# Performance work log

Measured on AMD Instinct MI355X. Metric: run time of the kernel, lower is better.

Reference implementation:

```python
import jax, jax.numpy as jnp
import numpy as np

N_ITER = 64   # projected-subgradient iterations of the batched DRO QP solver
LR0 = 0.05    # base step size (diminishing 1/sqrt(t))


def project_simplex(v):
    # Euclidean projection onto {z >= 0, sum z = 1} (sort-based, O(n log n))
    n = v.shape[0]
    u = jnp.sort(v)[::-1]
    css = jnp.cumsum(u) - 1.0
    k = jnp.arange(1, n + 1, dtype=v.dtype)
    cond = (u - css / k) > 0          # prefix-true pattern
    idx = jnp.sum(cond.astype(jnp.int32)) - 1
    theta = jnp.take(css, idx) / jnp.take(k, idx)
    return jnp.maximum(v - theta, 0.0)


def _dro_obj(z, c, lam, ep, y_hat, rho):
    # Tractable TV-DRO counterpart (Ben-Tal et al. 2013) with eta and obj_aux
    # eliminated analytically:
    #   obj_i* = max(-lam, u_i - eta),  u_i = (ep_i.z - c)^2
    #   feasibility: eta >= max_i u_i - lam; objective nondecreasing in eta
    #   => eta* = max_i u_i - lam
    s = ep @ z - c                     # (n_obs,)
    u = s * s
    umax = jnp.max(u)
    inner = jnp.mean(jnp.maximum(-lam, u - umax + lam))
    return (umax - lam) + rho * lam + inner - jnp.dot(y_hat, z)


_grad_obj = jax.grad(_dro_obj, argnums=(0, 1, 2))


def _solve_one(y_hat, ep, rho):
    # Projected subgradient descent on (z in simplex, c free, lam >= 0)
    n_y = y_hat.shape[0]
    z0 = jnp.full((n_y,), 1.0 / n_y, y_hat.dtype)
    c0 = jnp.mean(ep @ z0)
    lam0 = jnp.asarray(1.0, y_hat.dtype)

    def step(carry, t):
        z, c, lam = carry
        gz, gc, glam = _grad_obj(z, c, lam, ep, y_hat, rho)
        lr = LR0 / jnp.sqrt(t + 1.0)
        z = project_simplex(z - lr * gz)
        c = c - lr * gc
        lam = jnp.maximum(lam - lr * glam, 0.0)
        return (z, c, lam), None

    (z, _, _), _ = jax.lax.scan(step, (z0, c0, lam0),
                                jnp.arange(N_ITER, dtype=y_hat.dtype))
    return z


def setup_inputs() -> dict:
    key = jax.random.key(0)
    kx, ky, kw, kb = jax.random.split(key, 4)
    n_obs, n_x, n_y = 2048, 128, 64
    X = jax.random.normal(kx, (n_obs, n_x), jnp.float32)
    Y = jax.random.normal(ky, (n_obs, n_y), jnp.float32)
    W = jax.random.normal(kw, (n_y, n_x), jnp.float32) / np.sqrt(n_x).astype(np.float32)
    b = jax.random.normal(kb, (n_y,), jnp.float32) * 0.01
    rho = jnp.array([0.1], jnp.float32)
    return {"X": X, "Y": Y, "rho": rho, "W": W, "b": b}


def reference(X, Y, rho, W, b):
    # prediction layer: per-sample linear predict (vectorized over n_obs)
    Y_hat = X @ W.T + b                        # (n_obs, n_y)
    ep = Y - Y_hat                             # residuals, shared by all solves
    # batched DRO solve: one convex problem per scenario y_hat_t (vmapped)
    Z_star = jax.vmap(lambda yh: _solve_one(yh, ep, rho[0]))(Y_hat)
    Z_star = jax.lax.stop_gradient(Z_star)     # torch code detaches z_t
    return Z_star, Y_hat
```

## Files before the change

### kernel.cpp

```cpp
#include <hip/hip_runtime.h>

#define NOBS 2048
#define NX   128
#define NY   64
#define BS   8
#define NT   1024
#define NWAVE (NT / 64)
#define NITER 64

template <int CTRL>
__device__ __forceinline__ float dpp_f(float x) {
    return __int_as_float(__builtin_amdgcn_update_dpp(
        0, __float_as_int(x), CTRL, 0xf, 0xf, true));
}
__device__ __forceinline__ float wave_sum64(float v) {
    v += dpp_f<0x111>(v);
    v += dpp_f<0x112>(v);
    v += dpp_f<0x114>(v);
    v += dpp_f<0x118>(v);
    v += dpp_f<0x142>(v);
    v += dpp_f<0x143>(v);
    return v;
}
__device__ __forceinline__ float wave_max64_nonneg(float v) {
    v = fmaxf(v, dpp_f<0x111>(v));
    v = fmaxf(v, dpp_f<0x112>(v));
    v = fmaxf(v, dpp_f<0x114>(v));
    v = fmaxf(v, dpp_f<0x118>(v));
    v = fmaxf(v, dpp_f<0x142>(v));
    v = fmaxf(v, dpp_f<0x143>(v));
    return v;
}

__global__ __launch_bounds__(256) void prep_kernel(
    const float* __restrict__ X, const float* __restrict__ Y,
    const float* __restrict__ W, const float* __restrict__ b,
    float* __restrict__ yhat_out, float* __restrict__ ep, float* __restrict__ epsum)
{
    __shared__ float Xs[4][NX];
    const int t = threadIdx.x;
    const int row0 = blockIdx.x * 4;
    for (int f = t; f < 4 * NX; f += 256)
        Xs[f >> 7][f & 127] = X[(row0 + (f >> 7)) * NX + (f & 127)];
    __syncthreads();

    const int k = t & 63;
    const int r = t >> 6;
    const float4* W4 = reinterpret_cast<const float4*>(W + k * NX);
    const float4* X4 = reinterpret_cast<const float4*>(&Xs[r][0]);
    float acc = 0.f;
    #pragma unroll
    for (int x = 0; x < NX / 4; ++x) {
        float4 wv = W4[x];
        float4 xv = X4[x];
        acc += wv.x * xv.x + wv.y * xv.y + wv.z * xv.z + wv.w * xv.w;
    }
    const float yh = acc + b[k];
    const int i = row0 + r;
    yhat_out[i * NY + k] = yh;
    const float e = Y[i * NY + k] - yh;
    ep[i * NY + k] = e;

    float se = wave_sum64(e);
    if ((t & 63) == 63) atomicAdd(epsum, se);
}

__global__ __launch_bounds__(NT, 4) void solve_kernel(
    const float* __restrict__ ep, const float* __restrict__ yhat,
    const float* __restrict__ epsum, const float* __restrict__ rho_p,
    float* __restrict__ zout)
{
    __shared__ float Zs[BS][NY];
    __shared__ float Yh[BS][NY];
    __shared__ float V[NOBS][BS];
    __shared__ float Rpart[NWAVE][NY][BS];
    __shared__ float Rr[NY][BS];
    __shared__ float redBuf[NWAVE][32];
    __shared__ float scal[32];
    __shared__ float umaxS[BS], cS[BS], lamS[BS], gcS[BS], glamS[BS], wAS[BS];

    const int t = threadIdx.x;
    const int lane = t & 63;
    const int wv = t >> 6;
    const int sc0 = blockIdx.x * BS;
    const float rho = rho_p[0];

    if (t < BS * NY) {
        const int j = t >> 6, k = t & 63;
        Yh[j][k] = yhat[(sc0 + j) * NY + k];
        Zs[j][k] = 1.0f / 64.0f;
    }
    if (t < BS) {
        cS[t] = epsum[0] * (1.0f / 131072.0f);
        lamS[t] = 1.0f;
    }
    __syncthreads();

    const int i0 = t;
    const int i1 = t + NT;
    const float4* ep4 = reinterpret_cast<const float4*>(ep);

    for (int it = 0; it < NITER; ++it) {
        const float lr = 0.05f / sqrtf((float)it + 1.0f);

        float s0[BS], s1[BS];
        #pragma unroll
        for (int j = 0; j < BS; ++j) { s0[j] = 0.f; s1[j] = 0.f; }
        #pragma unroll 4
        for (int k4 = 0; k4 < NY / 4; ++k4) {
            const float4 ea = ep4[i0 * (NY / 4) + k4];
            const float4 eb = ep4[i1 * (NY / 4) + k4];
            #pragma unroll
            for (int j = 0; j < BS; ++j) {
                const float4 zv = *reinterpret_cast<const float4*>(&Zs[j][k4 * 4]);
                s0[j] += ea.x * zv.x + ea.y * zv.y + ea.z * zv.z + ea.w * zv.w;
                s1[j] += eb.x * zv.x + eb.y * zv.y + eb.z * zv.z + eb.w * zv.w;
            }
        }
        float lamR[BS];
        #pragma unroll
        for (int j = 0; j < BS; ++j) {
            const float cj = cS[j];
            lamR[j] = lamS[j];
            s0[j] -= cj; s1[j] -= cj;
        }

        #pragma unroll
        for (int j = 0; j < BS; ++j) {
            float pm = fmaxf(s0[j] * s0[j], s1[j] * s1[j]);
            pm = wave_max64_nonneg(pm);
            if (lane == 63) redBuf[wv][j] = pm;
        }
        __syncthreads();
        if (t < BS) {
            float m = redBuf[0][t];
            #pragma unroll
            for (int w = 1; w < NWAVE; ++w) m = fmaxf(m, redBuf[w][t]);
            umaxS[t] = m;
        }
        __syncthreads();

        #pragma unroll
        for (int j = 0; j < BS; ++j) {
            const float um = umaxS[j], lm = lamR[j];
            float pa = 0.f, pe = 0.f, pas = 0.f, pes = 0.f;
            {
                const float s = s0[j], u = s * s;
                const float x = (u - um) + lm;
                const float a = (x > -lm) ? 1.0f : ((x == -lm) ? 0.5f : 0.0f);
                const float e = (u == um) ? 1.0f : 0.0f;
                pa += a; pe += e; pas += a * s; pes += e * s;
            }
            {
                const float s = s1[j], u = s * s;
                const float x = (u - um) + lm;
                const float a = (x > -lm) ? 1.0f : ((x == -lm) ? 0.5f : 0.0f);
                const float e = (u == um) ? 1.0f : 0.0f;
                pa += a; pe += e; pas += a * s; pes += e * s;
            }
            pa = wave_sum64(pa); pe = wave_sum64(pe);
            pas = wave_sum64(pas); pes = wave_sum64(pes);
            if (lane == 63) {
                redBuf[wv][j] = pa;       redBuf[wv][8 + j] = pe;
                redBuf[wv][16 + j] = pas; redBuf[wv][24 + j] = pes;
            }
        }
        __syncthreads();
        if (t < 32) {
            float ssum = 0.f;
            #pragma unroll
            for (int w = 0; w < NWAVE; ++w) ssum += redBuf[w][t];
            scal[t] = ssum;
        }
        __syncthreads();
        if (t < BS) {
            const int j = t;
            const float sumA = scal[j], sumEq = scal[8 + j];
            const float sumAS = scal[16 + j], sumEqS = scal[24 + j];
            const float abar = sumA * (1.0f / (float)NOBS);
            const float wA = (1.0f - abar) / sumEq;
            wAS[j] = wA;
            gcS[j] = -2.0f * (sumAS * (1.0f / (float)NOBS) + wA * sumEqS);
            glamS[j] = (rho - 2.0f) + 2.0f * abar;
        }
        __syncthreads();

        {
            float v0[BS], v1[BS];
            #pragma unroll
            for (int j = 0; j < BS; ++j) {
                const float um = umaxS[j], lm = lamR[j], wA = wAS[j];
                {
                    const float s = s0[j], u = s * s;
                    const float x = (u - um) + lm;
                    const float a = (x > -lm) ? 1.0f : ((x == -lm) ? 0.5f : 0.0f);
                    const float e = (u == um) ? 1.0f : 0.0f;
                    v0[j] = (a * (1.0f / (float)NOBS) + e * wA) * s;
                }
                {
                    const float s = s1[j], u = s * s;
                    const float x = (u - um) + lm;
                    const float a = (x > -lm) ? 1.0f : ((x == -lm) ? 0.5f : 0.0f);
                    const float e = (u == um) ? 1.0f : 0.0f;
                    v1[j] = (a * (1.0f / (float)NOBS) + e * wA) * s;
                }
            }
            *reinterpret_cast<float4*>(&V[i0][0]) = make_float4(v0[0], v0[1], v0[2], v0[3]);
            *reinterpret_cast<float4*>(&V[i0][4]) = make_float4(v0[4], v0[5], v0[6], v0[7]);
            *reinterpret_cast<float4*>(&V[i1][0]) = make_float4(v1[0], v1[1], v1[2], v1[3]);
            *reinterpret_cast<float4*>(&V[i1][4]) = make_float4(v1[4], v1[5], v1[6], v1[7]);
        }
        __syncthreads();

        {
            float rp[BS];
            #pragma unroll
            for (int j = 0; j < BS; ++j) rp[j] = 0.f;
            const int ibeg = wv * (NOBS / NWAVE);
            #pragma unroll 4
            for (int ii = 0; ii < NOBS / NWAVE; ++ii) {
                const int i = ibeg + ii;
                const float e = ep[i * NY + lane];
                const float4 va = *reinterpret_cast<const float4*>(&V[i][0]);
                const float4 vb = *reinterpret_cast<const float4*>(&V[i][4]);
                rp[0] += e * va.x; rp[1] += e * va.y; rp[2] += e * va.z; rp[3] += e * va.w;
                rp[4] += e * vb.x; rp[5] += e * vb.y; rp[6] += e * vb.z; rp[7] += e * vb.w;
            }
            *reinterpret_cast<float4*>(&Rpart[wv][lane][0]) = make_float4(rp[0], rp[1], rp[2], rp[3]);
            *reinterpret_cast<float4*>(&Rpart[wv][lane][4]) = make_float4(rp[4], rp[5], rp[6], rp[7]);
        }
        __syncthreads();
        if (t < NY * BS) {
            const int k = t >> 3, j = t & 7;
            float ssum = 0.f;
            #pragma unroll
            for (int w = 0; w < NWAVE; ++w) ssum += Rpart[w][k][j];
            Rr[k][j] = ssum;
        }
        __syncthreads();

        if (wv < BS) {
            const int j = wv, k = lane;
            const float r = Rr[k][j];
            const float gz = 2.0f * r - Yh[j][k];
            const float vz = Zs[j][k] - lr * gz;

            float sv = vz;
            #pragma unroll
            for (int sz = 2; sz <= 64; sz <<= 1) {
                #pragma unroll
                for (int st = sz >> 1; st > 0; st >>= 1) {
                    const float other = __shfl_xor(sv, st, 64);
                    const bool desc = ((lane & sz) == 0);
                    const bool lower = ((lane & st) == 0);
                    const float mx = fmaxf(sv, other), mn = fminf(sv, other);
                    sv = (lower == desc) ? mx : mn;
                }
            }
            float css = sv;
            #pragma unroll
            for (int off = 1; off < 64; off <<= 1) {
                const float nb = __shfl_up(css, off, 64);
                if (lane >= off) css += nb;
            }
            css -= 1.0f;
            const bool cond = (sv - css / (float)(lane + 1)) > 0.0f;
            const unsigned long long bal = __ballot(cond);
            const int idx = __popcll(bal) - 1;
            const float cssIdx = __shfl(css, idx, 64);
            const float theta = cssIdx / (float)(idx + 1);
            Zs[j][k] = fmaxf(vz - theta, 0.0f);
            if (lane == 0) {
                cS[j] = cS[j] - lr * gcS[j];
                lamS[j] = fmaxf(lamS[j] - lr * glamS[j], 0.0f);
            }
        }
        __syncthreads();
    }

    if (t < BS * NY) {
        const int j = t >> 6, k = t & 63;
        zout[(sc0 + j) * NY + k] = Zs[j][k];
    }
}

extern "C" void kernel_launch(void* const* d_in, const int* in_sizes, int n_in,
                              void* d_out, int out_size, void* d_ws, size_t ws_size,
                              hipStream_t stream) {
    const float* X   = (const float*)d_in[0];
    const float* Y   = (const float*)d_in[1];
    const float* rho = (const float*)d_in[2];
    const float* W   = (const float*)d_in[3];
    const float* b   = (const float*)d_in[4];

    float* out   = (float*)d_out;
    float* zout  = out;
    float* yhat  = out + NOBS * NY;
    float* ep    = (float*)d_ws;
    float* epsum = ep + NOBS * NY;

    hipMemsetAsync(epsum, 0, sizeof(float), stream);
    prep_kernel<<<NOBS / 4, 256, 0, stream>>>(X, Y, W, b, yhat, ep, epsum);
    solve_kernel<<<NOBS / BS, NT, 0, stream>>>(ep, yhat, epsum, rho, zout);
}
```

Baseline: 2.162 ms.

## Use LDS atomics for block reductions and register-tile the ep^T·V gradient

Per-wave max and sum partials now go straight into shared accumulators through LDS atomicMax/atomicAdd, which removes two barriers and the serial cross-wave reduction passes in each iteration. Every thread recomputes wA from the shared sums itself, and the accumulators are reset during the Rr reduction phase. The ep^T·V gradient loop is restructured so each lane loads float4 ep rows and keeps 4x8 accumulators, and partials are combined with cross-lane shuffles. z and y_hat stay in registers for the projection step. The changes add register pressure and rely on the atomic float-as-int max being valid for non-negative values.

Result: slower. 5.667 ms (+162.1%).

```diff
diff --git a/kernel.cpp b/kernel.cpp
--- a/kernel.cpp
+++ b/kernel.cpp
@@ -70,14 +70,13 @@
     const float* __restrict__ epsum, const float* __restrict__ rho_p,
     float* __restrict__ zout)
 {
-    __shared__ float Zs[BS][NY];
-    __shared__ float Yh[BS][NY];
     __shared__ float V[NOBS][BS];
     __shared__ float Rpart[NWAVE][NY][BS];
     __shared__ float Rr[NY][BS];
-    __shared__ float redBuf[NWAVE][32];
+    __shared__ float Zs[BS][NY];
     __shared__ float scal[32];
-    __shared__ float umaxS[BS], cS[BS], lamS[BS], gcS[BS], glamS[BS], wAS[BS];
+    __shared__ int   umaxI[BS];
+    __shared__ float cS[BS], lamS[BS], gcS[BS], glamS[BS];
 
     const int t = threadIdx.x;
     const int lane = t & 63;
@@ -85,12 +84,14 @@
     const int sc0 = blockIdx.x * BS;
     const float rho = rho_p[0];
 
-    if (t < BS * NY) {
-        const int j = t >> 6, k = t & 63;
-        Yh[j][k] = yhat[(sc0 + j) * NY + k];
-        Zs[j][k] = 1.0f / 64.0f;
-    }
+    float zReg = 1.0f / 64.0f;
+    float yhReg = 0.0f;
+    if (wv < BS) yhReg = yhat[(sc0 + wv) * NY + lane];
+
+    if (t < BS * NY) Zs[t >> 6][t & 63] = 1.0f / 64.0f;
+    if (t < 32) scal[t] = 0.0f;
     if (t < BS) {
+        umaxI[t] = 0;
         cS[t] = epsum[0] * (1.0f / 131072.0f);
         lamS[t] = 1.0f;
     }
@@ -99,6 +100,8 @@
     const int i0 = t;
     const int i1 = t + NT;
     const float4* ep4 = reinterpret_cast<const float4*>(ep);
+    const float4* epA = ep4 + i0 * (NY / 4);
+    const float4* epB = ep4 + i1 * (NY / 4);
 
     for (int it = 0; it < NITER; ++it) {
         const float lr = 0.05f / sqrtf((float)it + 1.0f);
@@ -108,8 +111,8 @@
         for (int j = 0; j < BS; ++j) { s0[j] = 0.f; s1[j] = 0.f; }
         #pragma unroll 4
         for (int k4 = 0; k4 < NY / 4; ++k4) {
-            const float4 ea = ep4[i0 * (NY / 4) + k4];
-            const float4 eb = ep4[i1 * (NY / 4) + k4];
+            const float4 ea = epA[k4];
+            const float4 eb = epB[k4];
             #pragma unroll
             for (int j = 0; j < BS; ++j) {
                 const float4 zv = *reinterpret_cast<const float4*>(&Zs[j][k4 * 4]);
@@ -129,80 +132,71 @@
         for (int j = 0; j < BS; ++j) {
             float pm = fmaxf(s0[j] * s0[j], s1[j] * s1[j]);
             pm = wave_max64_nonneg(pm);
-            if (lane == 63) redBuf[wv][j] = pm;
-        }
-        __syncthreads();
-        if (t < BS) {
-            float m = redBuf[0][t];
-            #pragma unroll
-            for (int w = 1; w < NWAVE; ++w) m = fmaxf(m, redBuf[w][t]);
-            umaxS[t] = m;
-        }
-        __syncthreads();
+            if (lane == 63) atomicMax(&umaxI[j], __float_as_int(pm));
+        }
+        __syncthreads();
+
+        float um[BS];
+        #pragma unroll
+        for (int j = 0; j < BS; ++j) um[j] = __int_as_float(umaxI[j]);
 
         #pragma unroll
         for (int j = 0; j < BS; ++j) {
-            const float um = umaxS[j], lm = lamR[j];
-            float pa = 0.f, pe = 0.f, pas = 0.f, pes = 0.f;
+            const float umj = um[j], lm = lamR[j];
+            float pa, pe, pas, pes;
             {
                 const float s = s0[j], u = s * s;
-                const float x = (u - um) + lm;
+                const float x = (u - umj) + lm;
                 const float a = (x > -lm) ? 1.0f : ((x == -lm) ? 0.5f : 0.0f);
-                const float e = (u == um) ? 1.0f : 0.0f;
-                pa += a; pe += e; pas += a * s; pes += e * s;
+                const float e = (u == umj) ? 1.0f : 0.0f;
+                pa = a; pe = e; pas = a * s; pes = e * s;
             }
             {
                 const float s = s1[j], u = s * s;
-                const float x = (u - um) + lm;
+                const float x = (u - umj) + lm;
                 const float a = (x > -lm) ? 1.0f : ((x == -lm) ? 0.5f : 0.0f);
-                const float e = (u == um) ? 1.0f : 0.0f;
+                const float e = (u == umj) ? 1.0f : 0.0f;
                 pa += a; pe += e; pas += a * s; pes += e * s;
             }
             pa = wave_sum64(pa); pe = wave_sum64(pe);
             pas = wave_sum64(pas); pes = wave_sum64(pes);
             if (lane == 63) {
-                redBuf[wv][j] = pa;       redBuf[wv][8 + j] = pe;
-                redBuf[wv][16 + j] = pas; redBuf[wv][24 + j] = pes;
-            }
-        }
-        __syncthreads();
-        if (t < 32) {
-            float ssum = 0.f;
-            #pragma unroll
-            for (int w = 0; w < NWAVE; ++w) ssum += redBuf[w][t];
-            scal[t] = ssum;
-        }
-        __syncthreads();
+                atomicAdd(&scal[j], pa);       atomicAdd(&scal[8 + j], pe);
+                atomicAdd(&scal[16 + j], pas); atomicAdd(&scal[24 + j], pes);
+            }
+        }
+        __syncthreads();
+
+        float wA[BS];
+        #pragma unroll
+        for (int j = 0; j < BS; ++j) {
+            const float abar = scal[j] * (1.0f / (float)NOBS);
+            wA[j] = (1.0f - abar) / scal[8 + j];
+        }
         if (t < BS) {
-            const int j = t;
-            const float sumA = scal[j], sumEq = scal[8 + j];
-            const float sumAS = scal[16 + j], sumEqS = scal[24 + j];
-            const float abar = sumA * (1.0f / (float)NOBS);
-            const float wA = (1.0f - abar) / sumEq;
-            wAS[j] = wA;
-            gcS[j] = -2.0f * (sumAS * (1.0f / (float)NOBS) + wA * sumEqS);
-            glamS[j] = (rho - 2.0f) + 2.0f * abar;
-        }
-        __syncthreads();
-
+            const float abar = scal[t] * (1.0f / (float)NOBS);
+            const float wAt = (1.0f - abar) / scal[8 + t];
+            gcS[t] = -2.0f * (scal[16 + t] * (1.0f / (float)NOBS) + wAt * scal[24 + t]);
+            glamS[t] = (rho - 2.0f) + 2.0f * abar;
+        }
         {
             float v0[BS], v1[BS];
             #pragma unroll
             for (int j = 0; j < BS; ++j) {
-                const float um = umaxS[j], lm = lamR[j], wA = wAS[j];
+                const float umj = um[j], lm = lamR[j], wAj = wA[j];
                 {
                     const float s = s0[j], u = s * s;
-                    const float x = (u - um) + lm;
+                    const float x = (u - umj) + lm;
                     const float a = (x > -lm) ? 1.0f : ((x == -lm) ? 0.5f : 0.0f);
-                    const float e = (u == um) ? 1.0f : 0.0f;
-                    v0[j] = (a * (1.0f / (float)NOBS) + e * wA) * s;
+                    const float e = (u == umj) ? 1.0f : 0.0f;
+                    v0[j] = (a * (1.0f / (float)NOBS) + e * wAj) * s;
                 }
                 {
                     const float s = s1[j], u = s * s;
-                    const float x = (u - um) + lm;
+                    const float x = (u - umj) + lm;
                     const float a = (x > -lm) ? 1.0f : ((x == -lm) ? 0.5f : 0.0f);
-                    const float e = (u == um) ? 1.0f : 0.0f;
-                    v1[j] = (a * (1.0f / (float)NOBS) + e * wA) * s;
+                    const float e = (u == umj) ? 1.0f : 0.0f;
+                    v1[j] = (a * (1.0f / (float)NOBS) + e * wAj) * s;
                 }
             }
             *reinterpret_cast<float4*>(&V[i0][0]) = make_float4(v0[0], v0[1], v0[2], v0[3]);
@@ -213,37 +207,71 @@
         __syncthreads();
 
         {
-            float rp[BS];
-            #pragma unroll
-            for (int j = 0; j < BS; ++j) rp[j] = 0.f;
-            const int ibeg = wv * (NOBS / NWAVE);
-            #pragma unroll 4
-            for (int ii = 0; ii < NOBS / NWAVE; ++ii) {
-                const int i = ibeg + ii;
-                const float e = ep[i * NY + lane];
-                const float4 va = *reinterpret_cast<const float4*>(&V[i][0]);
-                const float4 vb = *reinterpret_cast<const float4*>(&V[i][4]);
-                rp[0] += e * va.x; rp[1] += e * va.y; rp[2] += e * va.z; rp[3] += e * va.w;
-                rp[4] += e * vb.x; rp[5] += e * vb.y; rp[6] += e * vb.z; rp[7] += e * vb.w;
-            }
-            *reinterpret_cast<float4*>(&Rpart[wv][lane][0]) = make_float4(rp[0], rp[1], rp[2], rp[3]);
-            *reinterpret_cast<float4*>(&Rpart[wv][lane][4]) = make_float4(rp[4], rp[5], rp[6], rp[7]);
-        }
-        __syncthreads();
+            const int sub = lane >> 4;
+            const int kq  = lane & 15;
+            float rp0[BS], rp1[BS], rp2[BS], rp3[BS];
+            #pragma unroll
+            for (int j = 0; j < BS; ++j) { rp0[j] = 0.f; rp1[j] = 0.f; rp2[j] = 0.f; rp3[j] = 0.f; }
+
+            const int rbase = wv * (NOBS / NWAVE) + sub;
+            const float4* vp = reinterpret_cast<const float4*>(&V[rbase][0]);
+            #pragma unroll
+            for (int c8 = 0; c8 < 8; ++c8) {
+                const float4* epc = ep4 + (rbase + c8 * 16) * (NY / 4) + kq;
+                #pragma unroll
+                for (int u = 0; u < 4; ++u) {
+                    const int ii = c8 * 4 + u;
+                    const float4 e4 = epc[u * 64];
+                    const float4 va = vp[ii * 8];
+                    const float4 vb = vp[ii * 8 + 1];
+                    rp0[0] += e4.x * va.x; rp0[1] += e4.x * va.y; rp0[2] += e4.x * va.z; rp0[3] += e4.x * va.w;
+                    rp0[4] += e4.x * vb.x; rp0[5] += e4.x * vb.y; rp0[6] += e4.x * vb.z; rp0[7] += e4.x * vb.w;
+                    rp1[0] += e4.y * va.x; rp1[1] += e4.y * va.y; rp1[2] += e4.y * va.z; rp1[3] += e4.y * va.w;
+                    rp1[4] += e4.y * vb.x; rp1[5] += e4.y * vb.y; rp1[6] += e4.y * vb.z; rp1[7] += e4.y * vb.w;
+                    rp2[0] += e4.z * va.x; rp2[1] += e4.z * va.y; rp2[2] += e4.z * va.z; rp2[3] += e4.z * va.w;
+                    rp2[4] += e4.z * vb.x; rp2[5] += e4.z * vb.y; rp2[6] += e4.z * vb.z; rp2[7] += e4.z * vb.w;
+                    rp3[0] += e4.w * va.x; rp3[1] += e4.w * va.y; rp3[2] += e4.w * va.z; rp3[3] += e4.w * va.w;
+                    rp3[4] += e4.w * vb.x; rp3[5] += e4.w * vb.y; rp3[6] += e4.w * vb.z; rp3[7] += e4.w * vb.w;
+                }
+            }
+            #pragma unroll
+            for (int j = 0; j < BS; ++j) {
+                float a0 = rp0[j]; a0 += __shfl_xor(a0, 16, 64); a0 += __shfl_xor(a0, 32, 64); rp0[j] = a0;
+                float a1 = rp1[j]; a1 += __shfl_xor(a1, 16, 64); a1 += __shfl_xor(a1, 32, 64); rp1[j] = a1;
+                float a2 = rp2[j]; a2 += __shfl_xor(a2, 16, 64); a2 += __shfl_xor(a2, 32, 64); rp2[j] = a2;
+                float a3 = rp3[j]; a3 += __shfl_xor(a3, 16, 64); a3 += __shfl_xor(a3, 32, 64); rp3[j] = a3;
+            }
+            float w[BS];
+            #pragma unroll
+            for (int j = 0; j < BS; ++j) {
+                const float t01 = (sub & 1) ? rp1[j] : rp0[j];
+                const float t23 = (sub & 1) ? rp3[j] : rp2[j];
+                w[j] = (sub & 2) ? t23 : t01;
+            }
+            float* dst = &Rpart[wv][4 * kq + sub][0];
+            *reinterpret_cast<float4*>(dst)     = make_float4(w[0], w[1], w[2], w[3]);
+            *reinterpret_cast<float4*>(dst + 4) = make_float4(w[4], w[5], w[6], w[7]);
+        }
+        __syncthreads();
+
         if (t < NY * BS) {
             const int k = t >> 3, j = t & 7;
             float ssum = 0.f;
             #pragma unroll
             for (int w = 0; w < NWAVE; ++w) ssum += Rpart[w][k][j];
             Rr[k][j] = ssum;
+        } else if (t < NY * BS + 32) {
+            scal[t - NY * BS] = 0.0f;
+        } else if (t < NY * BS + 32 + BS) {
+            umaxI[t - NY * BS - 32] = 0;
         }
         __syncthreads();
 
         if (wv < BS) {
             const int j = wv, k = lane;
             const float r = Rr[k][j];
-            const float gz = 2.0f * r - Yh[j][k];
-            const float vz = Zs[j][k] - lr * gz;
+            const float gz = 2.0f * r - yhReg;
+            const float vz = zReg - lr * gz;
 
             float sv = vz;
             #pragma unroll
@@ -269,7 +297,8 @@
             const int idx = __popcll(bal) - 1;
             const float cssIdx = __shfl(css, idx, 64);
             const float theta = cssIdx / (float)(idx + 1);
-            Zs[j][k] = fmaxf(vz - theta, 0.0f);
+            zReg = fmaxf(vz - theta, 0.0f);
+            Zs[j][k] = zReg;
             if (lane == 0) {
                 cS[j] = cS[j] - lr * gcS[j];
                 lamS[j] = fmaxf(lamS[j] - lr * glamS[j], 0.0f);
@@ -278,10 +307,7 @@
         __syncthreads();
     }
 
-    if (t < BS * NY) {
-        const int j = t >> 6, k = t & 63;
-        zout[(sc0 + j) * NY + k] = Zs[j][k];
-    }
+    if (wv < BS) zout[(sc0 + wv) * NY + lane] = zReg;
 }
 
 extern "C" void kernel_launch(void* const* d_in, const int* in_sizes, int n_in,
```
